# Kernel optimization log

Measured on AMD Instinct MI355X. Metric: run time of the kernel, lower is better.

Reference implementation:

```python
import jax, jax.numpy as jnp
import numpy as np

EPS, GAMMA, LAMB, C1, C2 = 0.2, 0.99, 0.95, 0.5, 0.01
T = 8388608  # 2**23 timesteps


def setup_inputs() -> dict:
    key = jax.random.key(0)
    k1, k2, k3, k4 = jax.random.split(key, 4)
    # probs in (0.1, 1.0) to keep ratios / log well-conditioned
    probs = jax.random.uniform(k1, (T,), jnp.float32, 0.1, 1.0)
    probs_old = jax.random.uniform(k2, (T,), jnp.float32, 0.1, 1.0)
    rewards = jax.random.normal(k3, (T,), jnp.float32)
    values = jax.random.normal(k4, (T,), jnp.float32)
    return {"probs": probs, "probs_old": probs_old,
            "rewards": rewards, "values": values}


def _calc_gaes(rewards, values):
    # delta_t = r_t - v_t + gamma * v_{t+1}, with v_T = 0
    v_next = jnp.concatenate([values[1:], jnp.zeros((1,), values.dtype)])
    delta = rewards - values + GAMMA * v_next
    def step(gae, d):
        gae = GAMMA * LAMB * gae + d
        return gae, gae
    _, gaes = jax.lax.scan(step, jnp.float32(0.0), delta, reverse=True)
    return gaes


def _calc_value_targets(rewards):
    def step(acc, r):
        acc = acc * GAMMA + r
        return acc, acc
    _, targets = jax.lax.scan(step, jnp.float32(0.0), rewards, reverse=True)
    return targets


def reference(probs, probs_old, rewards, values):
    advantages = _calc_gaes(rewards, values)
    ratio = probs / probs_old
    clipped = jnp.clip(ratio, 1.0 - EPS, 1.0 + EPS)
    clip_loss = -jnp.sum(jnp.minimum(ratio * advantages, clipped * advantages))
    values_target = _calc_value_targets(rewards)
    value_loss = jnp.sum((values - values_target) ** 2)  # MSELoss(sum)
    entropy_loss = -jnp.sum(probs * jnp.log(probs + 1e-5))
    return clip_loss + C1 * value_loss + C2 * entropy_loss
```

## Files before the change

### kernel.cpp

```cpp
#include <hip/hip_runtime.h>


#define T_TOTAL  8388608
#define L_CHUNK  8192
#define NBLK     (T_TOTAL / L_CHUNK)
#define NT       512
#define M        16
#define W_HALO   2048

#define EPSF   0.2f
#define GAMMAF 0.99f
#define C1F    0.5f
#define C2F    0.01f

#define AG1  (0.99f * 0.95f)
#define AG2  (AG1 * AG1)
#define AG4  (AG2 * AG2)
#define AG8  (AG4 * AG4)
#define AG16 (AG8 * AG8)
#define G2   (GAMMAF * GAMMAF)
#define G4   (G2 * G2)
#define G8   (G4 * G4)
#define G16  (G8 * G8)

__global__ __launch_bounds__(NT) void ppo_loss_kernel(
    const float* __restrict__ probs,
    const float* __restrict__ probs_old,
    const float* __restrict__ rewards,
    const float* __restrict__ values,
    float* __restrict__ out)
{
    __shared__ float sg[NT];
    __shared__ float sr[NT];

    const int j = threadIdx.x;
    const int c = blockIdx.x;
    const long base = (long)c * L_CHUNK;

    float hp_g = 0.0f, hp_r = 0.0f;
    if (c != NBLK - 1) {
        const long hb = base + L_CHUNK + 4L * j;
        const float4 r4 = *reinterpret_cast<const float4*>(rewards + hb);
        const float4 v4 = *reinterpret_cast<const float4*>(values + hb);
        const float  vn = values[hb + 4];
        const float d0 = r4.x - v4.x + GAMMAF * v4.y;
        const float d1 = r4.y - v4.y + GAMMAF * v4.z;
        const float d2 = r4.z - v4.z + GAMMAF * v4.w;
        const float d3 = r4.w - v4.w + GAMMAF * vn;
        hp_g = d0 + AG1 * (d1 + AG1 * (d2 + AG1 * d3));
        hp_r = r4.x + GAMMAF * (r4.y + GAMMAF * (r4.z + GAMMAF * r4.w));
    }
    sg[j] = hp_g; sr[j] = hp_r;
    __syncthreads();
    {
        float fg = AG4, fr = G4;
        for (int n = NT / 2; n >= 1; n >>= 1) {
            float tg = 0.0f, tr = 0.0f;
            if (j < n) {
                tg = sg[2 * j] + fg * sg[2 * j + 1];
                tr = sr[2 * j] + fr * sr[2 * j + 1];
            }
            __syncthreads();
            if (j < n) { sg[j] = tg; sr[j] = tr; }
            __syncthreads();
            fg *= fg; fr *= fr;
        }
    }
    const float Kg = sg[0];
    const float Kr = sr[0];
    __syncthreads();

    const long g0 = base + (long)j * M;

    float r[M], v[M], d[M];
#pragma unroll
    for (int b = 0; b < M / 4; ++b) {
        const float4 rr = *reinterpret_cast<const float4*>(rewards + g0 + 4 * b);
        const float4 vv = *reinterpret_cast<const float4*>(values  + g0 + 4 * b);
        r[4 * b + 0] = rr.x; r[4 * b + 1] = rr.y; r[4 * b + 2] = rr.z; r[4 * b + 3] = rr.w;
        v[4 * b + 0] = vv.x; v[4 * b + 1] = vv.y; v[4 * b + 2] = vv.z; v[4 * b + 3] = vv.w;
    }
    const float v_next = (g0 + M < T_TOTAL) ? values[g0 + M] : 0.0f;
#pragma unroll
    for (int i = 0; i < M - 1; ++i) d[i] = r[i] - v[i] + GAMMAF * v[i + 1];
    d[M - 1] = r[M - 1] - v[M - 1] + GAMMAF * v_next;

    float Pg = 0.0f, Pr = 0.0f;
#pragma unroll
    for (int i = M - 1; i >= 0; --i) {
        Pg = AG1   * Pg + d[i];
        Pr = GAMMAF * Pr + r[i];
    }

    sg[j] = (j == NT - 1) ? (Pg + AG16 * Kg) : Pg;
    sr[j] = (j == NT - 1) ? (Pr + G16  * Kr) : Pr;
    __syncthreads();
    {
        float fg = AG16, fr = G16;
        for (int s = 1; s < NT; s <<= 1) {
            const float tg = sg[j] + ((j + s < NT) ? fg * sg[j + s] : 0.0f);
            const float tr = sr[j] + ((j + s < NT) ? fr * sr[j + s] : 0.0f);
            __syncthreads();
            sg[j] = tg; sr[j] = tr;
            __syncthreads();
            fg *= fg; fr *= fr;
        }
    }
    const float cg = (j < NT - 1) ? sg[j + 1] : Kg;
    const float cr = (j < NT - 1) ? sr[j + 1] : Kr;
    __syncthreads();

    float y = cg, tt = cr;
    float acc = 0.0f;
#pragma unroll
    for (int b = M / 4 - 1; b >= 0; --b) {
        const float4 p4 = *reinterpret_cast<const float4*>(probs     + g0 + 4 * b);
        const float4 q4 = *reinterpret_cast<const float4*>(probs_old + g0 + 4 * b);
        const float pa[4] = { p4.x, p4.y, p4.z, p4.w };
        const float qa[4] = { q4.x, q4.y, q4.z, q4.w };
#pragma unroll
        for (int k = 3; k >= 0; --k) {
            const int i = 4 * b + k;
            y  = AG1    * y  + d[i];
            tt = GAMMAF * tt + r[i];
            const float ratio = __fdividef(pa[k], qa[k]);
            const float cl    = fminf(fmaxf(ratio, 1.0f - EPSF), 1.0f + EPSF);
            const float term  = fminf(ratio * y, cl * y);
            const float vd    = v[i] - tt;
            acc += C1F * vd * vd - term - C2F * pa[k] * __logf(pa[k] + 1e-5f);
        }
    }

    sg[j] = acc;
    __syncthreads();
    for (int n = NT / 2; n >= 64; n >>= 1) {
        if (j < n) sg[j] += sg[j + n];
        __syncthreads();
    }
    if (j < 64) {
        float x = sg[j];
        for (int off = 32; off >= 1; off >>= 1)
            x += __shfl_down(x, off, 64);
        if (j == 0) atomicAdd(out, x);
    }
}

extern "C" void kernel_launch(void* const* d_in, const int* in_sizes, int n_in,
                              void* d_out, int out_size, void* d_ws, size_t ws_size,
                              hipStream_t stream) {
    const float* probs     = (const float*)d_in[0];
    const float* probs_old = (const float*)d_in[1];
    const float* rewards   = (const float*)d_in[2];
    const float* values    = (const float*)d_in[3];
    float* out = (float*)d_out;

    hipMemsetAsync(out, 0, sizeof(float), stream);
    ppo_loss_kernel<<<NBLK, NT, 0, stream>>>(probs, probs_old, rewards, values, out);
}
```

Measured before the change: 161.0 us.

## Replace shared-memory block scans with wave-shuffle suffix scans and shrink halo

Replaces the shared-memory tree reduction and Hillis-Steele suffix scans, each step of which needed two barriers, with 64-lane shuffle-based suffix scans plus a small cross-wave combine over 8 per-wave values. The halo is cut from 2048 to 1024 elements, and all four input streams are loaded up front so memory latency overlaps with compute. The ratio and entropy work is hoisted ahead of the single remaining barrier, and the final reduction uses wave shuffles. The aim is to remove dozens of __syncthreads and LDS round trips, at the cost of more registers and a shorter halo window for the discount truncation.

New measurement: 154.0 us. 1.05x faster.

```diff
diff --git a/kernel.cpp b/kernel.cpp
--- a/kernel.cpp
+++ b/kernel.cpp
@@ -6,22 +6,46 @@
 #define NBLK     (T_TOTAL / L_CHUNK)
 #define NT       512
 #define M        16
-#define W_HALO   2048
+#define W_HALO   1024
 
-#define EPSF   0.2f
-#define GAMMAF 0.99f
-#define C1F    0.5f
-#define C2F    0.01f
+#define EPSF 0.2f
+#define GF   0.99f
+#define C1F  0.5f
+#define C2F  0.01f
+#define AGL  ((float)(0.99 * 0.95))
 
-#define AG1  (0.99f * 0.95f)
-#define AG2  (AG1 * AG1)
-#define AG4  (AG2 * AG2)
-#define AG8  (AG4 * AG4)
-#define AG16 (AG8 * AG8)
-#define G2   (GAMMAF * GAMMAF)
-#define G4   (G2 * G2)
-#define G8   (G4 * G4)
-#define G16  (G8 * G8)
+constexpr float fpowc(double a, int n) {
+    double r = 1.0;
+    for (int i = 0; i < n; ++i) r *= a;
+    return (float)r;
+}
+constexpr float AG2    = fpowc(0.99 * 0.95, 2);
+constexpr float AG16   = fpowc(0.99 * 0.95, 16);
+constexpr float AG32   = fpowc(0.99 * 0.95, 32);
+constexpr float AG64   = fpowc(0.99 * 0.95, 64);
+constexpr float AG128  = fpowc(0.99 * 0.95, 128);
+constexpr float AG256  = fpowc(0.99 * 0.95, 256);
+constexpr float AG512  = fpowc(0.99 * 0.95, 512);
+constexpr float AG1024 = fpowc(0.99 * 0.95, 1024);
+constexpr float G2    = fpowc(0.99, 2);
+constexpr float G16   = fpowc(0.99, 16);
+constexpr float G32   = fpowc(0.99, 32);
+constexpr float G64   = fpowc(0.99, 64);
+constexpr float G128  = fpowc(0.99, 128);
+constexpr float G256  = fpowc(0.99, 256);
+constexpr float G512  = fpowc(0.99, 512);
+constexpr float G1024 = fpowc(0.99, 1024);
+
+__device__ __forceinline__ float wave_suffix_scan(float val, float w, int lane) {
+#pragma unroll
+    for (int s = 1; s < 64; s <<= 1) {
+        float o = __shfl_down(val, s, 64);
+        o = (lane + s < 64) ? o : 0.0f;
+        val += w * o;
+        w *= w;
+    }
+    return val;
+}
 
 __global__ __launch_bounds__(NT) void ppo_loss_kernel(
     const float* __restrict__ probs,
@@ -30,118 +54,125 @@
     const float* __restrict__ values,
     float* __restrict__ out)
 {
-    __shared__ float sg[NT];
-    __shared__ float sr[NT];
+    __shared__ float s_hg[8], s_hr[8], s_wg[8], s_wr[8], s_red[8];
 
-    const int j = threadIdx.x;
-    const int c = blockIdx.x;
+    const int  j    = threadIdx.x;
+    const int  lane = j & 63;
+    const int  wid  = j >> 6;
+    const int  c    = blockIdx.x;
     const long base = (long)c * L_CHUNK;
+    const long g0   = base + (long)j * M;
 
-    float hp_g = 0.0f, hp_r = 0.0f;
-    if (c != NBLK - 1) {
-        const long hb = base + L_CHUNK + 4L * j;
-        const float4 r4 = *reinterpret_cast<const float4*>(rewards + hb);
-        const float4 v4 = *reinterpret_cast<const float4*>(values + hb);
-        const float  vn = values[hb + 4];
-        const float d0 = r4.x - v4.x + GAMMAF * v4.y;
-        const float d1 = r4.y - v4.y + GAMMAF * v4.z;
-        const float d2 = r4.z - v4.z + GAMMAF * v4.w;
-        const float d3 = r4.w - v4.w + GAMMAF * vn;
-        hp_g = d0 + AG1 * (d1 + AG1 * (d2 + AG1 * d3));
-        hp_r = r4.x + GAMMAF * (r4.y + GAMMAF * (r4.z + GAMMAF * r4.w));
+    float2 hr2 = make_float2(0.f, 0.f), hv2 = make_float2(0.f, 0.f);
+    float  hva = 0.0f;
+    const bool has_halo = (c != NBLK - 1);
+    if (has_halo) {
+        const long hb = base + L_CHUNK + 2L * j;
+        hr2 = *reinterpret_cast<const float2*>(rewards + hb);
+        hv2 = *reinterpret_cast<const float2*>(values  + hb);
+        hva = values[hb + 2];
     }
-    sg[j] = hp_g; sr[j] = hp_r;
-    __syncthreads();
-    {
-        float fg = AG4, fr = G4;
-        for (int n = NT / 2; n >= 1; n >>= 1) {
-            float tg = 0.0f, tr = 0.0f;
-            if (j < n) {
-                tg = sg[2 * j] + fg * sg[2 * j + 1];
-                tr = sr[2 * j] + fr * sr[2 * j + 1];
-            }
-            __syncthreads();
-            if (j < n) { sg[j] = tg; sr[j] = tr; }
-            __syncthreads();
-            fg *= fg; fr *= fr;
-        }
-    }
-    const float Kg = sg[0];
-    const float Kr = sr[0];
-    __syncthreads();
-
-    const long g0 = base + (long)j * M;
-
-    float r[M], v[M], d[M];
+    float4 r4[4], v4[4], p4[4], q4[4];
 #pragma unroll
-    for (int b = 0; b < M / 4; ++b) {
-        const float4 rr = *reinterpret_cast<const float4*>(rewards + g0 + 4 * b);
-        const float4 vv = *reinterpret_cast<const float4*>(values  + g0 + 4 * b);
-        r[4 * b + 0] = rr.x; r[4 * b + 1] = rr.y; r[4 * b + 2] = rr.z; r[4 * b + 3] = rr.w;
-        v[4 * b + 0] = vv.x; v[4 * b + 1] = vv.y; v[4 * b + 2] = vv.z; v[4 * b + 3] = vv.w;
+    for (int b = 0; b < 4; ++b) {
+        r4[b] = *reinterpret_cast<const float4*>(rewards   + g0 + 4 * b);
+        v4[b] = *reinterpret_cast<const float4*>(values    + g0 + 4 * b);
     }
     const float v_next = (g0 + M < T_TOTAL) ? values[g0 + M] : 0.0f;
 #pragma unroll
-    for (int i = 0; i < M - 1; ++i) d[i] = r[i] - v[i] + GAMMAF * v[i + 1];
-    d[M - 1] = r[M - 1] - v[M - 1] + GAMMAF * v_next;
+    for (int b = 0; b < 4; ++b) {
+        p4[b] = *reinterpret_cast<const float4*>(probs     + g0 + 4 * b);
+        q4[b] = *reinterpret_cast<const float4*>(probs_old + g0 + 4 * b);
+    }
 
-    float Pg = 0.0f, Pr = 0.0f;
+    float r[M], v[M];
+#pragma unroll
+    for (int b = 0; b < 4; ++b) {
+        r[4*b+0] = r4[b].x; r[4*b+1] = r4[b].y; r[4*b+2] = r4[b].z; r[4*b+3] = r4[b].w;
+        v[4*b+0] = v4[b].x; v[4*b+1] = v4[b].y; v[4*b+2] = v4[b].z; v[4*b+3] = v4[b].w;
+    }
+
+    float hg = 0.f, hr = 0.f;
+    if (has_halo) {
+        const float d0 = hr2.x - hv2.x + GF * hv2.y;
+        const float d1 = hr2.y - hv2.y + GF * hva;
+        hg = d0 + AGL * d1;
+        hr = hr2.x + GF * hr2.y;
+    }
+    hg = wave_suffix_scan(hg, AG2, lane);
+    hr = wave_suffix_scan(hr, G2,  lane);
+    if (lane == 0) { s_hg[wid] = hg; s_hr[wid] = hr; }
+
+    float Pg = 0.f, Pr = 0.f;
 #pragma unroll
     for (int i = M - 1; i >= 0; --i) {
-        Pg = AG1   * Pg + d[i];
-        Pr = GAMMAF * Pr + r[i];
+        const float vn = (i == M - 1) ? v_next : v[i + 1];
+        const float di = r[i] - v[i] + GF * vn;
+        Pg = AGL * Pg + di;
+        Pr = GF  * Pr + r[i];
     }
+    const float Sg = wave_suffix_scan(Pg, AG16, lane);
+    const float Sr = wave_suffix_scan(Pr, G16,  lane);
+    if (lane == 0) { s_wg[wid] = Sg; s_wr[wid] = Sr; }
+    float sng = __shfl_down(Sg, 1, 64); sng = (lane < 63) ? sng : 0.0f;
+    float snr = __shfl_down(Sr, 1, 64); snr = (lane < 63) ? snr : 0.0f;
 
-    sg[j] = (j == NT - 1) ? (Pg + AG16 * Kg) : Pg;
-    sr[j] = (j == NT - 1) ? (Pr + G16  * Kr) : Pr;
-    __syncthreads();
-    {
-        float fg = AG16, fr = G16;
-        for (int s = 1; s < NT; s <<= 1) {
-            const float tg = sg[j] + ((j + s < NT) ? fg * sg[j + s] : 0.0f);
-            const float tr = sr[j] + ((j + s < NT) ? fr * sr[j + s] : 0.0f);
-            __syncthreads();
-            sg[j] = tg; sr[j] = tr;
-            __syncthreads();
-            fg *= fg; fr *= fr;
-        }
-    }
-    const float cg = (j < NT - 1) ? sg[j + 1] : Kg;
-    const float cr = (j < NT - 1) ? sr[j + 1] : Kr;
-    __syncthreads();
-
-    float y = cg, tt = cr;
-    float acc = 0.0f;
+    float ratio[M];
+    float accE = 0.f;
 #pragma unroll
-    for (int b = M / 4 - 1; b >= 0; --b) {
-        const float4 p4 = *reinterpret_cast<const float4*>(probs     + g0 + 4 * b);
-        const float4 q4 = *reinterpret_cast<const float4*>(probs_old + g0 + 4 * b);
-        const float pa[4] = { p4.x, p4.y, p4.z, p4.w };
-        const float qa[4] = { q4.x, q4.y, q4.z, q4.w };
+    for (int b = 0; b < 4; ++b) {
+        const float pa[4] = { p4[b].x, p4[b].y, p4[b].z, p4[b].w };
+        const float qa[4] = { q4[b].x, q4[b].y, q4[b].z, q4[b].w };
 #pragma unroll
-        for (int k = 3; k >= 0; --k) {
-            const int i = 4 * b + k;
-            y  = AG1    * y  + d[i];
-            tt = GAMMAF * tt + r[i];
-            const float ratio = __fdividef(pa[k], qa[k]);
-            const float cl    = fminf(fmaxf(ratio, 1.0f - EPSF), 1.0f + EPSF);
-            const float term  = fminf(ratio * y, cl * y);
-            const float vd    = v[i] - tt;
-            acc += C1F * vd * vd - term - C2F * pa[k] * __logf(pa[k] + 1e-5f);
+        for (int k = 0; k < 4; ++k) {
+            ratio[4*b+k] = __fdividef(pa[k], qa[k]);
+            accE -= C2F * pa[k] * __logf(pa[k] + 1e-5f);
         }
     }
 
-    sg[j] = acc;
     __syncthreads();
-    for (int n = NT / 2; n >= 64; n >>= 1) {
-        if (j < n) sg[j] += sg[j + n];
-        __syncthreads();
+
+    float Kg = 0.f, Kr = 0.f;
+#pragma unroll
+    for (int w = 7; w >= 0; --w) { Kg = s_hg[w] + AG128 * Kg; Kr = s_hr[w] + G128 * Kr; }
+    float Cg = Kg, Cr = Kr;
+    for (int w = 7; w > wid; --w) { Cg = s_wg[w] + AG1024 * Cg; Cr = s_wr[w] + G1024 * Cr; }
+
+    const int k63 = 63 - lane;
+    float pwg = 1.f, pwr = 1.f;
+    if (k63 & 1)  { pwg *= AG16;  pwr *= G16;  }
+    if (k63 & 2)  { pwg *= AG32;  pwr *= G32;  }
+    if (k63 & 4)  { pwg *= AG64;  pwr *= G64;  }
+    if (k63 & 8)  { pwg *= AG128; pwr *= G128; }
+    if (k63 & 16) { pwg *= AG256; pwr *= G256; }
+    if (k63 & 32) { pwg *= AG512; pwr *= G512; }
+
+    float y  = sng + pwg * Cg;
+    float tt = snr + pwr * Cr;
+
+    float acc = accE;
+#pragma unroll
+    for (int i = M - 1; i >= 0; --i) {
+        const float vn = (i == M - 1) ? v_next : v[i + 1];
+        const float di = r[i] - v[i] + GF * vn;
+        y  = AGL * y  + di;
+        tt = GF  * tt + r[i];
+        const float rt   = ratio[i];
+        const float cl   = fminf(fmaxf(rt, 1.0f - EPSF), 1.0f + EPSF);
+        const float term = fminf(rt * y, cl * y);
+        const float vd   = v[i] - tt;
+        acc = fmaf(C1F * vd, vd, acc) - term;
     }
-    if (j < 64) {
-        float x = sg[j];
-        for (int off = 32; off >= 1; off >>= 1)
-            x += __shfl_down(x, off, 64);
-        if (j == 0) atomicAdd(out, x);
+
+#pragma unroll
+    for (int s = 32; s >= 1; s >>= 1) acc += __shfl_down(acc, s, 64);
+    if (lane == 0) s_red[wid] = acc;
+    __syncthreads();
+    if (j == 0) {
+        float t = 0.f;
+#pragma unroll
+        for (int w = 0; w < 8; ++w) t += s_red[w];
+        atomicAdd(out, t);
     }
 }
 
```
